# Performance work log

Hardware: AMD Instinct MI355X
Metric: run time of the kernel (lower is better)

The kernel has to match this reference:

```python
import jax, jax.numpy as jnp
import numpy as np

N_QUBITS = 4
DIM = 2 ** N_QUBITS  # 16
BATCH = 2 ** 21


def setup_inputs() -> dict:
    key = jax.random.key(0)
    k1, k2 = jax.random.split(key)
    x = jax.random.normal(k1, (BATCH, DIM), dtype=jnp.float32)
    q_weights = jax.random.normal(k2, (N_QUBITS,), dtype=jnp.float32)
    return {"x": x, "q_weights": q_weights}


def _pauli_z_signs():
    # wire 0 is the most-significant bit in default.qubit's amplitude ordering
    idx = jnp.arange(DIM)
    cols = [1.0 - 2.0 * ((idx >> (N_QUBITS - 1 - i)) & 1) for i in range(N_QUBITS)]
    return jnp.stack(cols, axis=1).astype(jnp.float32)  # [16, 4]


def reference(x, q_weights):
    # NaN scrub + reshape, as in the original call()
    x = jnp.where(jnp.isnan(x), jnp.zeros_like(x), x).reshape(-1, DIM)
    # AmplitudeEmbedding(normalize=True): per-sample L2 normalization
    norm = jnp.sqrt(jnp.sum(x * x, axis=1, keepdims=True))
    state = (x / norm).astype(jnp.complex64)
    B = state.shape[0]
    state = state.reshape((B,) + (2,) * N_QUBITS)  # [B,2,2,2,2]
    half = q_weights.astype(jnp.float32) * 0.5
    c, s = jnp.cos(half), jnp.sin(half)
    # RX(theta) = [[cos(t/2), -i sin(t/2)], [-i sin(t/2), cos(t/2)]], applied per wire
    for i in range(N_QUBITS):
        U = jnp.stack([
            jnp.stack([c[i] + 0j, -1j * s[i]]),
            jnp.stack([-1j * s[i], c[i] + 0j]),
        ]).astype(jnp.complex64)  # [2,2]
        axis = 1 + i
        state = jnp.moveaxis(jnp.tensordot(state, U, axes=[[axis], [1]]), -1, axis)
    probs = (state.real ** 2 + state.imag ** 2).reshape(B, DIM)  # [B,16]
    # <Z_i> = sum_k p_k * (+1 if bit_i(k)==0 else -1)
    return probs @ _pauli_z_signs()  # [B, n_qubits]
```

## Files before the change

kernel.cpp:

```cpp
#include <hip/hip_runtime.h>


constexpr int BLOCK = 256;
constexpr int MAX_BLOCKS = 2048;

typedef float fvec4 __attribute__((ext_vector_type(4)));

__global__ __launch_bounds__(BLOCK) void quantum_z_kernel(
    const float* __restrict__ x,
    const float* __restrict__ w,
    float* __restrict__ out,
    int n_vec4)
{
    const int j0 = threadIdx.x & 3;
    const float cw = cosf(w[j0]);

    const int stride = gridDim.x * BLOCK;
    for (int gid = blockIdx.x * BLOCK + threadIdx.x; gid < n_vec4; gid += stride) {
        int j = gid & 3;

        fvec4 v = reinterpret_cast<const fvec4*>(x)[gid];

        float a = (v.x != v.x) ? 0.0f : v.x;
        float b = (v.y != v.y) ? 0.0f : v.y;
        float c = (v.z != v.z) ? 0.0f : v.z;
        float d = (v.w != v.w) ? 0.0f : v.w;

        float p0 = a * a, p1 = b * b, p2 = c * c, p3 = d * d;
        float q  = (p0 + p1) + (p2 + p3);
        float t2 = p2 + p3;
        float t3 = p1 + p3;

        float r1   = __shfl_xor(q, 1);
        float pair = q + r1;
        float oddq = (j & 1) ? q : r1;
        float r2   = __shfl_xor(pair, 2);
        float SS   = pair + r2;
        float S0   = (j & 2) ? pair : r2;
        float S1   = oddq + __shfl_xor(oddq, 2);
        float S2   = t2 + __shfl_xor(t2, 1);
        S2 += __shfl_xor(S2, 2);
        float S3   = t3 + __shfl_xor(t3, 1);
        S3 += __shfl_xor(S3, 2);

        float Sj = (j & 2) ? ((j & 1) ? S3 : S2) : ((j & 1) ? S1 : S0);
        float z  = cw * (1.0f - 2.0f * Sj / SS);
        __builtin_nontemporal_store(z, out + gid);
    }
}

extern "C" void kernel_launch(void* const* d_in, const int* in_sizes, int n_in,
                              void* d_out, int out_size, void* d_ws, size_t ws_size,
                              hipStream_t stream) {
    const float* x = (const float*)d_in[0];
    const float* w = (const float*)d_in[1];
    float* out = (float*)d_out;

    int n_vec4 = in_sizes[0] / 4;
    int grid = (n_vec4 + BLOCK - 1) / BLOCK;
    if (grid > MAX_BLOCKS) grid = MAX_BLOCKS;
    hipLaunchKernelGGL(quantum_z_kernel, dim3(grid), dim3(BLOCK), 0, stream,
                       x, w, out, n_vec4);
}
```

Measured before the change: 197.0 us.

## Map one sample per thread and drop cross-lane shuffle reductions

Each thread now handles a whole 16-amplitude sample instead of one float4 quarter of it. It does four nontemporal float4 loads, computes the four Z expectations locally with no wavefront shuffles, and writes one float4 of output. This removes the shuffle and select overhead and puts more bytes in flight per thread. In exchange, each load instruction is strided by 64 bytes across lanes, so coalescing per instruction is worse and it relies on the cache to combine accesses.

```diff
diff --git a/kernel.cpp b/kernel.cpp
--- a/kernel.cpp
+++ b/kernel.cpp
@@ -6,46 +6,54 @@
 
 typedef float fvec4 __attribute__((ext_vector_type(4)));
 
+__device__ __forceinline__ void squares(fvec4 v, float& q, float& t2, float& t3) {
+    float a = (v.x != v.x) ? 0.0f : v.x;
+    float b = (v.y != v.y) ? 0.0f : v.y;
+    float c = (v.z != v.z) ? 0.0f : v.z;
+    float d = (v.w != v.w) ? 0.0f : v.w;
+    float p0 = a * a, p1 = b * b, p2 = c * c, p3 = d * d;
+    t2 = p2 + p3;
+    t3 = p1 + p3;
+    q  = (p0 + p1) + t2;
+}
+
 __global__ __launch_bounds__(BLOCK) void quantum_z_kernel(
     const float* __restrict__ x,
     const float* __restrict__ w,
     float* __restrict__ out,
-    int n_vec4)
+    int n_samples)
 {
-    const int j0 = threadIdx.x & 3;
-    const float cw = cosf(w[j0]);
+    const float cw0 = cosf(w[0]), cw1 = cosf(w[1]);
+    const float cw2 = cosf(w[2]), cw3 = cosf(w[3]);
 
     const int stride = gridDim.x * BLOCK;
-    for (int gid = blockIdx.x * BLOCK + threadIdx.x; gid < n_vec4; gid += stride) {
-        int j = gid & 3;
+    for (int s = blockIdx.x * BLOCK + threadIdx.x; s < n_samples; s += stride) {
+        const fvec4* xp = reinterpret_cast<const fvec4*>(x) + (size_t)s * 4;
+        fvec4 v0 = __builtin_nontemporal_load(xp + 0);
+        fvec4 v1 = __builtin_nontemporal_load(xp + 1);
+        fvec4 v2 = __builtin_nontemporal_load(xp + 2);
+        fvec4 v3 = __builtin_nontemporal_load(xp + 3);
 
-        fvec4 v = reinterpret_cast<const fvec4*>(x)[gid];
+        float q0, t20, t30, q1, t21, t31, q2, t22, t32, q3, t23, t33;
+        squares(v0, q0, t20, t30);
+        squares(v1, q1, t21, t31);
+        squares(v2, q2, t22, t32);
+        squares(v3, q3, t23, t33);
 
-        float a = (v.x != v.x) ? 0.0f : v.x;
-        float b = (v.y != v.y) ? 0.0f : v.y;
-        float c = (v.z != v.z) ? 0.0f : v.z;
-        float d = (v.w != v.w) ? 0.0f : v.w;
+        float SS = (q0 + q1) + (q2 + q3);
+        float S0 = q2 + q3;
+        float S1 = q1 + q3;
+        float S2 = (t20 + t21) + (t22 + t23);
+        float S3 = (t30 + t31) + (t32 + t33);
 
-        float p0 = a * a, p1 = b * b, p2 = c * c, p3 = d * d;
-        float q  = (p0 + p1) + (p2 + p3);
-        float t2 = p2 + p3;
-        float t3 = p1 + p3;
+        float inv2 = -2.0f / SS;
+        fvec4 o;
+        o.x = cw0 * __builtin_fmaf(S0, inv2, 1.0f);
+        o.y = cw1 * __builtin_fmaf(S1, inv2, 1.0f);
+        o.z = cw2 * __builtin_fmaf(S2, inv2, 1.0f);
+        o.w = cw3 * __builtin_fmaf(S3, inv2, 1.0f);
 
-        float r1   = __shfl_xor(q, 1);
-        float pair = q + r1;
-        float oddq = (j & 1) ? q : r1;
-        float r2   = __shfl_xor(pair, 2);
-        float SS   = pair + r2;
-        float S0   = (j & 2) ? pair : r2;
-        float S1   = oddq + __shfl_xor(oddq, 2);
-        float S2   = t2 + __shfl_xor(t2, 1);
-        S2 += __shfl_xor(S2, 2);
-        float S3   = t3 + __shfl_xor(t3, 1);
-        S3 += __shfl_xor(S3, 2);
-
-        float Sj = (j & 2) ? ((j & 1) ? S3 : S2) : ((j & 1) ? S1 : S0);
-        float z  = cw * (1.0f - 2.0f * Sj / SS);
-        __builtin_nontemporal_store(z, out + gid);
+        __builtin_nontemporal_store(o, reinterpret_cast<fvec4*>(out) + s);
     }
 }
 
@@ -56,9 +64,9 @@
     const float* w = (const float*)d_in[1];
     float* out = (float*)d_out;
 
-    int n_vec4 = in_sizes[0] / 4;
-    int grid = (n_vec4 + BLOCK - 1) / BLOCK;
+    int n_samples = in_sizes[0] / 16;
+    int grid = (n_samples + BLOCK - 1) / BLOCK;
     if (grid > MAX_BLOCKS) grid = MAX_BLOCKS;
     hipLaunchKernelGGL(quantum_z_kernel, dim3(grid), dim3(BLOCK), 0, stream,
-                       x, w, out, n_vec4);
+                       x, w, out, n_samples);
 }
```

After: 201.2 us. 2.2% more time.
